# Performance work log

Measured on AMD Instinct MI355X. Metric: run time of the kernel, lower is better.

## Reference

```python
import jax, jax.numpy as jnp
import numpy as np

DT = 0.01
OMEGA_MAX = 100.0


def setup_inputs() -> dict:
    key = jax.random.key(0)
    ks = jax.random.split(key, 7)
    B, T, D, M = 4, 4096, 1024, 64
    N = 2 * M
    u = jax.random.normal(ks[0], (B, T, D), dtype=jnp.float32)
    W_omega = jax.random.normal(ks[1], (M, D), dtype=jnp.float32) * 0.02
    b_omega = jnp.ones((M,), dtype=jnp.float32)
    W_zeta = jax.random.normal(ks[2], (M, D), dtype=jnp.float32) * 0.02
    b_zeta = jnp.zeros((M,), dtype=jnp.float32)
    W_B = jax.random.normal(ks[3], (N, D), dtype=jnp.float32) * (0.1 / np.sqrt(D))
    b_B = jnp.zeros((N,), dtype=jnp.float32)
    C = jax.random.normal(ks[4], (D, N), dtype=jnp.float32) * 0.01
    D_mat = jax.random.normal(ks[5], (D, D), dtype=jnp.float32) * 0.01
    return dict(u=u, W_omega=W_omega, b_omega=b_omega, W_zeta=W_zeta,
                b_zeta=b_zeta, W_B=W_B, b_B=b_B, C=C, D_mat=D_mat)


def reference(u, W_omega, b_omega, W_zeta, b_zeta, W_B, b_B, C, D_mat):
    B, T, D = u.shape
    M = W_omega.shape[0]
    # Hoist all per-step linear projections into batched GEMMs (same math).
    omega = jax.nn.softplus(jnp.einsum('btd,md->btm', u, W_omega) + b_omega)
    omega = jnp.clip(omega, 1e-4, OMEGA_MAX)                      # (B,T,M)
    zeta = jax.nn.sigmoid(jnp.einsum('btd,md->btm', u, W_zeta) + b_zeta)
    A = omega * omega                                             # (B,T,M)
    S = 1.0 / (1.0 + (DT * DT) * A)                               # (B,T,M)
    d = 1.0 - zeta                                                # (B,T,M)
    F = jnp.einsum('btd,nd->btn', u, W_B) + b_B                   # (B,T,2M)

    def step(x, inp):
        A_t, S_t, d_t, F_t = inp                                  # (B,M)x3, (B,2M)
        z = x[:, :M]
        y = x[:, M:]
        z_new = d_t * (S_t * z - DT * A_t * S_t * y)
        y_new = d_t * (DT * S_t * z + S_t * y)
        x_new = jnp.concatenate([z_new, y_new], axis=-1) + F_t
        return x_new, x_new

    x0 = jnp.zeros((B, 2 * M), dtype=u.dtype)
    tm = lambda a: jnp.swapaxes(a, 0, 1)  # to time-major for scan
    _, xs = jax.lax.scan(step, x0, (tm(A), tm(S), tm(d), tm(F)))
    xs = jnp.swapaxes(xs, 0, 1)                                   # (B,T,2M)
    # Output projection: y_t = x_t C^T + u_t D^T
    y = jnp.einsum('btn,dn->btd', xs, C) + jnp.einsum('bte,de->btd', u, D_mat)
    return y
```

## Files before the change

kernel.cpp:

```cpp
#include <hip/hip_runtime.h>
#include <hip/hip_bf16.h>
#include <math.h>

#define DTC 0.01f

typedef __attribute__((ext_vector_type(8))) short short8;
typedef __attribute__((ext_vector_type(4))) float f32x4;
typedef unsigned short bf16raw;

__device__ __forceinline__ bf16raw f2bf(float f){
  union { unsigned u; float f; } v; v.f = f;
  unsigned r = v.u + 0x7FFF + ((v.u >> 16) & 1u);
  return (bf16raw)(r >> 16);
}

__device__ __forceinline__ short8 ld8f(const float* __restrict__ p){
  float4 a = *(const float4*)p;
  float4 b = *(const float4*)(p + 4);
  short8 r;
  r[0] = (short)f2bf(a.x); r[1] = (short)f2bf(a.y);
  r[2] = (short)f2bf(a.z); r[3] = (short)f2bf(a.w);
  r[4] = (short)f2bf(b.x); r[5] = (short)f2bf(b.y);
  r[6] = (short)f2bf(b.z); r[7] = (short)f2bf(b.w);
  return r;
}

template<int ITERS>
__device__ __forceinline__ void stage_async(const bf16raw* __restrict__ src, long ld,
                                            long row0, int k0, bf16raw* lds,
                                            int wave, int lane){
#pragma unroll
  for (int i = 0; i < ITERS; ++i){
    int r0 = (wave*ITERS + i) * 16;
    long row = row0 + r0 + (lane >> 2);
    const bf16raw* gp = src + row*ld + k0 + (lane & 3)*8;
    bf16raw* lp = lds + r0*32;
    __builtin_amdgcn_global_load_lds((const __attribute__((address_space(1))) void*)gp,
                                     (__attribute__((address_space(3))) void*)lp,
                                     16, 0, 0);
  }
}

template<int NI>
__device__ __forceinline__ void mma_tile(const bf16raw* Alds, const bf16raw* Blds,
                                         f32x4 acc[4][NI], int wm, int wn, int quad, int t16){
  short8 af[4], bfr[NI];
#pragma unroll
  for (int mi = 0; mi < 4; ++mi)
    af[mi] = *(const short8*)(Alds + (wm*64 + mi*16 + t16)*32 + quad*8);
#pragma unroll
  for (int ni = 0; ni < NI; ++ni)
    bfr[ni] = *(const short8*)(Blds + (wn*(NI*16) + ni*16 + t16)*32 + quad*8);
#pragma unroll
  for (int mi = 0; mi < 4; ++mi)
#pragma unroll
    for (int ni = 0; ni < NI; ++ni)
      acc[mi][ni] = __builtin_amdgcn_mfma_f32_16x16x32_bf16(af[mi], bfr[ni], acc[mi][ni], 0, 0, 0);
}

extern "C" __global__ void k_prep(const float* __restrict__ u,
    const float* __restrict__ Wom, const float* __restrict__ Wze,
    const float* __restrict__ WB, const float* __restrict__ Cm,
    const float* __restrict__ Dm, bf16raw* __restrict__ u_bf,
    bf16raw* __restrict__ Wcat, bf16raw* __restrict__ C_bf,
    bf16raw* __restrict__ Dm_bf){
  long g = (long)blockIdx.x * 256 + threadIdx.x;
  const float* src; bf16raw* dst; long o;
  if      (g < 2097152){ src = u;   dst = u_bf;          o = g; }
  else if (g < 2105344){ src = Wom; dst = Wcat;          o = g - 2097152; }
  else if (g < 2113536){ src = Wze; dst = Wcat + 65536;  o = g - 2105344; }
  else if (g < 2129920){ src = WB;  dst = Wcat + 131072; o = g - 2113536; }
  else if (g < 2146304){ src = Cm;  dst = C_bf;          o = g - 2129920; }
  else                 { src = Dm;  dst = Dm_bf;         o = g - 2146304; }
  *(short8*)(dst + o*8) = ld8f(src + o*8);
}

extern "C" __global__ __launch_bounds__(256) void k_gemm_p(
    const bf16raw* __restrict__ u_bf, const bf16raw* __restrict__ Wcat,
    float* __restrict__ P){
  __shared__ __align__(16) bf16raw Alds[128*32];
  __shared__ __align__(16) bf16raw Blds[128*32];
  int tid = threadIdx.x, wave = tid >> 6, lane = tid & 63;
  int quad = lane >> 4, t16 = lane & 15;
  int wm = wave >> 1, wn = wave & 1;
  long row0 = (long)blockIdx.y * 128;
  int  col0 = blockIdx.x * 128;
  f32x4 acc[4][4] = {};
  for (int kt = 0; kt < 32; ++kt){
    __syncthreads();
    stage_async<2>(u_bf, 1024, row0, kt*32, Alds, wave, lane);
    stage_async<2>(Wcat, 1024, col0, kt*32, Blds, wave, lane);
    __syncthreads();
    mma_tile<4>(Alds, Blds, acc, wm, wn, quad, t16);
  }
#pragma unroll
  for (int mi = 0; mi < 4; ++mi)
#pragma unroll
    for (int ni = 0; ni < 4; ++ni)
#pragma unroll
      for (int r = 0; r < 4; ++r){
        long grow = row0 + wm*64 + mi*16 + quad*4 + r;
        int  gcol = col0 + wn*64 + ni*16 + t16;
        P[grow*256 + gcol] = acc[mi][ni][r];
      }
}

extern "C" __global__ __launch_bounds__(256, 2) void k_gemm_out(
    const bf16raw* __restrict__ Xs, const bf16raw* __restrict__ u_bf,
    const bf16raw* __restrict__ C_bf, const bf16raw* __restrict__ Dm_bf,
    float* __restrict__ out){
  __shared__ __align__(16) bf16raw Alds[128*32];
  __shared__ __align__(16) bf16raw Blds[256*32];
  int tid = threadIdx.x, wave = tid >> 6, lane = tid & 63;
  int quad = lane >> 4, t16 = lane & 15;
  int wm = wave >> 1, wn = wave & 1;
  long row0 = (long)blockIdx.y * 128;
  int  col0 = blockIdx.x * 256;
  f32x4 acc[4][8] = {};
  for (int kt = 0; kt < 4; ++kt){
    __syncthreads();
    stage_async<2>(Xs,   128, row0, kt*32, Alds, wave, lane);
    stage_async<4>(C_bf, 128, col0, kt*32, Blds, wave, lane);
    __syncthreads();
    mma_tile<8>(Alds, Blds, acc, wm, wn, quad, t16);
  }
  for (int kt = 0; kt < 32; ++kt){
    __syncthreads();
    stage_async<2>(u_bf,  1024, row0, kt*32, Alds, wave, lane);
    stage_async<4>(Dm_bf, 1024, col0, kt*32, Blds, wave, lane);
    __syncthreads();
    mma_tile<8>(Alds, Blds, acc, wm, wn, quad, t16);
  }
#pragma unroll
  for (int mi = 0; mi < 4; ++mi)
#pragma unroll
    for (int ni = 0; ni < 8; ++ni)
#pragma unroll
      for (int r = 0; r < 4; ++r){
        long grow = row0 + wm*64 + mi*16 + quad*4 + r;
        int  gcol = col0 + wn*128 + ni*16 + t16;
        out[grow*1024 + gcol] = acc[mi][ni][r];
      }
}

extern "C" __global__ void k_coef(const float* __restrict__ P,
    const float* __restrict__ b_om, const float* __restrict__ b_ze,
    const float* __restrict__ b_B, float4* __restrict__ Coef){
  int idx = blockIdx.x * 256 + threadIdx.x;
  int bt = idx >> 6, m = idx & 63;
  const float* row = P + (size_t)bt * 256;
  float wo = row[m]       + b_om[m];
  float wz = row[64 + m]  + b_ze[m];
  float fz = row[128 + m] + b_B[m];
  float fy = row[192 + m] + b_B[64 + m];
  float sp = (wo > 20.f) ? wo : log1pf(expf(wo));
  float omega = fminf(fmaxf(sp, 1e-4f), 100.f);
  float A = omega * omega;
  float S = 1.f / (1.f + DTC*DTC*A);
  float zeta = 1.f / (1.f + expf(-wz));
  float d = 1.f - zeta;
  float p = d * S;
  float q = p * DTC * A;
  Coef[idx] = make_float4(p, q, fz, fy);
}

extern "C" __global__ void k_scan1(const float4* __restrict__ Coef,
    float4* __restrict__ CM, float2* __restrict__ CV){
  int tid = threadIdx.x, c = blockIdx.x;
  int b = tid >> 6, m = tid & 63;
  const float4* cf = Coef + ((size_t)b*4096 + c*32)*64 + m;
  float m00=1.f, m01=0.f, m10=0.f, m11=0.f, vz=0.f, vy=0.f;
#pragma unroll 4
  for (int t = 0; t < 32; ++t){
    float4 f = cf[t*64];
    float p = f.x, q = f.y;
    float nvz = p*vz - q*vy + f.z;
    float nvy = DTC*p*vz + p*vy + f.w;
    vz = nvz; vy = nvy;
    float n00 = p*m00 - q*m10;
    float n01 = p*m01 - q*m11;
    float n10 = DTC*p*m00 + p*m10;
    float n11 = DTC*p*m01 + p*m11;
    m00=n00; m01=n01; m10=n10; m11=n11;
  }
  CM[c*256 + tid] = make_float4(m00, m01, m10, m11);
  CV[c*256 + tid] = make_float2(vz, vy);
}

extern "C" __global__ void k_scan2(const float4* __restrict__ CM,
    const float2* __restrict__ CV, float2* __restrict__ XIn){
  int tid = threadIdx.x;
  float xz = 0.f, xy = 0.f;
#pragma unroll 4
  for (int c = 0; c < 128; ++c){
    XIn[c*256 + tid] = make_float2(xz, xy);
    float4 Mv = CM[c*256 + tid];
    float2 Vv = CV[c*256 + tid];
    float nz = Mv.x*xz + Mv.y*xy + Vv.x;
    float ny = Mv.z*xz + Mv.w*xy + Vv.y;
    xz = nz; xy = ny;
  }
}

extern "C" __global__ void k_scan3(const float4* __restrict__ Coef,
    const float2* __restrict__ XIn, bf16raw* __restrict__ Xs){
  int tid = threadIdx.x, c = blockIdx.x;
  int b = tid >> 6, m = tid & 63;
  const float4* cf = Coef + ((size_t)b*4096 + c*32)*64 + m;
  float2 x0 = XIn[c*256 + tid];
  float xz = x0.x, xy = x0.y;
  bf16raw* xp = Xs + ((size_t)b*4096 + c*32)*128 + m;
#pragma unroll 4
  for (int t = 0; t < 32; ++t){
    float4 f = cf[t*64];
    float p = f.x, q = f.y;
    float nz = p*xz - q*xy + f.z;
    float ny = DTC*p*xz + p*xy + f.w;
    xz = nz; xy = ny;
    xp[t*128]      = f2bf(xz);
    xp[t*128 + 64] = f2bf(xy);
  }
}

extern "C" void kernel_launch(void* const* d_in, const int* in_sizes, int n_in,
                              void* d_out, int out_size, void* d_ws, size_t ws_size,
                              hipStream_t stream){
  const float* u   = (const float*)d_in[0];
  const float* Wom = (const float*)d_in[1];
  const float* bom = (const float*)d_in[2];
  const float* Wze = (const float*)d_in[3];
  const float* bze = (const float*)d_in[4];
  const float* WB  = (const float*)d_in[5];
  const float* bB  = (const float*)d_in[6];
  const float* Cm  = (const float*)d_in[7];
  const float* Dm  = (const float*)d_in[8];
  float* out = (float*)d_out;

  char* ws = (char*)d_ws;
  size_t off = 0;
  bf16raw* u_bf  = (bf16raw*)(ws + off); off += (size_t)16777216*2;
  bf16raw* Wcat  = (bf16raw*)(ws + off); off += (size_t)262144*2;
  bf16raw* C_bf  = (bf16raw*)(ws + off); off += (size_t)131072*2;
  bf16raw* Dm_bf = (bf16raw*)(ws + off); off += (size_t)1048576*2;
  float*   P     = (float*)  (ws + off);
  bf16raw* Xs    = (bf16raw*)P;
  off += (size_t)16384*256*4;
  float4*  Coef  = (float4*) (ws + off); off += (size_t)16384*64*16;
  float4*  CMw   = (float4*) (ws + off); off += (size_t)128*256*16;
  float2*  CVw   = (float2*) (ws + off); off += (size_t)128*256*8;
  float2*  XIn   = (float2*) (ws + off); off += (size_t)128*256*8;

  k_prep    <<<8896, 256, 0, stream>>>(u, Wom, Wze, WB, Cm, Dm, u_bf, Wcat, C_bf, Dm_bf);
  k_gemm_p  <<<dim3(2, 128), 256, 0, stream>>>(u_bf, Wcat, P);
  k_coef    <<<4096, 256, 0, stream>>>(P, bom, bze, bB, Coef);
  k_scan1   <<<128, 256, 0, stream>>>(Coef, CMw, CVw);
  k_scan2   <<<1, 256, 0, stream>>>(CMw, CVw, XIn);
  k_scan3   <<<128, 256, 0, stream>>>(Coef, XIn, Xs);
  k_gemm_out<<<dim3(4, 128), 256, 0, stream>>>(Xs, u_bf, C_bf, Dm_bf, out);
}
```

Measured before the change: 233.0 us.

## Fuse u conversion into projection GEMM, merge coef+scan1, parallelize chunk scan, retile output GEMM

```diff
diff --git a/kernel.cpp b/kernel.cpp
--- a/kernel.cpp
+++ b/kernel.cpp
@@ -58,26 +58,24 @@
       acc[mi][ni] = __builtin_amdgcn_mfma_f32_16x16x32_bf16(af[mi], bfr[ni], acc[mi][ni], 0, 0, 0);
 }
 
-extern "C" __global__ void k_prep(const float* __restrict__ u,
-    const float* __restrict__ Wom, const float* __restrict__ Wze,
-    const float* __restrict__ WB, const float* __restrict__ Cm,
-    const float* __restrict__ Dm, bf16raw* __restrict__ u_bf,
+extern "C" __global__ void k_prep(const float* __restrict__ Wom,
+    const float* __restrict__ Wze, const float* __restrict__ WB,
+    const float* __restrict__ Cm, const float* __restrict__ Dm,
     bf16raw* __restrict__ Wcat, bf16raw* __restrict__ C_bf,
     bf16raw* __restrict__ Dm_bf){
   long g = (long)blockIdx.x * 256 + threadIdx.x;
   const float* src; bf16raw* dst; long o;
-  if      (g < 2097152){ src = u;   dst = u_bf;          o = g; }
-  else if (g < 2105344){ src = Wom; dst = Wcat;          o = g - 2097152; }
-  else if (g < 2113536){ src = Wze; dst = Wcat + 65536;  o = g - 2105344; }
-  else if (g < 2129920){ src = WB;  dst = Wcat + 131072; o = g - 2113536; }
-  else if (g < 2146304){ src = Cm;  dst = C_bf;          o = g - 2129920; }
-  else                 { src = Dm;  dst = Dm_bf;         o = g - 2146304; }
+  if      (g <  8192){ src = Wom; dst = Wcat;          o = g; }
+  else if (g < 16384){ src = Wze; dst = Wcat + 65536;  o = g - 8192; }
+  else if (g < 32768){ src = WB;  dst = Wcat + 131072; o = g - 16384; }
+  else if (g < 49152){ src = Cm;  dst = C_bf;          o = g - 32768; }
+  else               { src = Dm;  dst = Dm_bf;         o = g - 49152; }
   *(short8*)(dst + o*8) = ld8f(src + o*8);
 }
 
 extern "C" __global__ __launch_bounds__(256) void k_gemm_p(
-    const bf16raw* __restrict__ u_bf, const bf16raw* __restrict__ Wcat,
-    float* __restrict__ P){
+    const float* __restrict__ u, const bf16raw* __restrict__ Wcat,
+    bf16raw* __restrict__ u_bf, float* __restrict__ P){
   __shared__ __align__(16) bf16raw Alds[128*32];
   __shared__ __align__(16) bf16raw Blds[128*32];
   int tid = threadIdx.x, wave = tid >> 6, lane = tid & 63;
@@ -85,11 +83,21 @@
   int wm = wave >> 1, wn = wave & 1;
   long row0 = (long)blockIdx.y * 128;
   int  col0 = blockIdx.x * 128;
+  int srow = tid >> 2, sk = (tid & 3) * 8;
+  bool writer = (blockIdx.x == 0);
   f32x4 acc[4][4] = {};
   for (int kt = 0; kt < 32; ++kt){
-    __syncthreads();
-    stage_async<2>(u_bf, 1024, row0, kt*32, Alds, wave, lane);
-    stage_async<2>(Wcat, 1024, col0, kt*32, Blds, wave, lane);
+    int k0 = kt*32;
+    short8 a0 = ld8f(u + (row0 + srow     )*1024 + k0 + sk);
+    short8 a1 = ld8f(u + (row0 + srow + 64)*1024 + k0 + sk);
+    __syncthreads();
+    *(short8*)(Alds + (srow     )*32 + sk) = a0;
+    *(short8*)(Alds + (srow + 64)*32 + sk) = a1;
+    stage_async<2>(Wcat, 1024, col0, k0, Blds, wave, lane);
+    if (writer){
+      *(short8*)(u_bf + (row0 + srow     )*1024 + k0 + sk) = a0;
+      *(short8*)(u_bf + (row0 + srow + 64)*1024 + k0 + sk) = a1;
+    }
     __syncthreads();
     mma_tile<4>(Alds, Blds, acc, wm, wn, quad, t16);
   }
@@ -105,101 +113,88 @@
       }
 }
 
-extern "C" __global__ __launch_bounds__(256, 2) void k_gemm_out(
-    const bf16raw* __restrict__ Xs, const bf16raw* __restrict__ u_bf,
-    const bf16raw* __restrict__ C_bf, const bf16raw* __restrict__ Dm_bf,
-    float* __restrict__ out){
-  __shared__ __align__(16) bf16raw Alds[128*32];
-  __shared__ __align__(16) bf16raw Blds[256*32];
-  int tid = threadIdx.x, wave = tid >> 6, lane = tid & 63;
-  int quad = lane >> 4, t16 = lane & 15;
-  int wm = wave >> 1, wn = wave & 1;
-  long row0 = (long)blockIdx.y * 128;
-  int  col0 = blockIdx.x * 256;
-  f32x4 acc[4][8] = {};
-  for (int kt = 0; kt < 4; ++kt){
-    __syncthreads();
-    stage_async<2>(Xs,   128, row0, kt*32, Alds, wave, lane);
-    stage_async<4>(C_bf, 128, col0, kt*32, Blds, wave, lane);
-    __syncthreads();
-    mma_tile<8>(Alds, Blds, acc, wm, wn, quad, t16);
-  }
-  for (int kt = 0; kt < 32; ++kt){
-    __syncthreads();
-    stage_async<2>(u_bf,  1024, row0, kt*32, Alds, wave, lane);
-    stage_async<4>(Dm_bf, 1024, col0, kt*32, Blds, wave, lane);
-    __syncthreads();
-    mma_tile<8>(Alds, Blds, acc, wm, wn, quad, t16);
-  }
-#pragma unroll
-  for (int mi = 0; mi < 4; ++mi)
-#pragma unroll
-    for (int ni = 0; ni < 8; ++ni)
-#pragma unroll
-      for (int r = 0; r < 4; ++r){
-        long grow = row0 + wm*64 + mi*16 + quad*4 + r;
-        int  gcol = col0 + wn*128 + ni*16 + t16;
-        out[grow*1024 + gcol] = acc[mi][ni][r];
-      }
-}
-
-extern "C" __global__ void k_coef(const float* __restrict__ P,
-    const float* __restrict__ b_om, const float* __restrict__ b_ze,
-    const float* __restrict__ b_B, float4* __restrict__ Coef){
-  int idx = blockIdx.x * 256 + threadIdx.x;
-  int bt = idx >> 6, m = idx & 63;
-  const float* row = P + (size_t)bt * 256;
-  float wo = row[m]       + b_om[m];
-  float wz = row[64 + m]  + b_ze[m];
-  float fz = row[128 + m] + b_B[m];
-  float fy = row[192 + m] + b_B[64 + m];
-  float sp = (wo > 20.f) ? wo : log1pf(expf(wo));
-  float omega = fminf(fmaxf(sp, 1e-4f), 100.f);
-  float A = omega * omega;
-  float S = 1.f / (1.f + DTC*DTC*A);
-  float zeta = 1.f / (1.f + expf(-wz));
-  float d = 1.f - zeta;
-  float p = d * S;
-  float q = p * DTC * A;
-  Coef[idx] = make_float4(p, q, fz, fy);
-}
-
-extern "C" __global__ void k_scan1(const float4* __restrict__ Coef,
-    float4* __restrict__ CM, float2* __restrict__ CV){
-  int tid = threadIdx.x, c = blockIdx.x;
-  int b = tid >> 6, m = tid & 63;
-  const float4* cf = Coef + ((size_t)b*4096 + c*32)*64 + m;
-  float m00=1.f, m01=0.f, m10=0.f, m11=0.f, vz=0.f, vy=0.f;
+extern "C" __global__ __launch_bounds__(256) void k_coefscan1(
+    const float* __restrict__ P, const float* __restrict__ b_om,
+    const float* __restrict__ b_ze, const float* __restrict__ b_B,
+    float4* __restrict__ Coef, float4* __restrict__ CMt,
+    float2* __restrict__ CVt){
+  __shared__ float4 lds_c[2048];
+  int tid = threadIdx.x;
+  int c = blockIdx.x;
+  int b = blockIdx.y;
+  int t = tid >> 3;
+  int m0 = (tid & 7) * 8;
+  long bt = (long)b*4096 + c*32 + t;
+  const float* row = P + bt*256;
+#pragma unroll
+  for (int j = 0; j < 8; ++j){
+    int m = m0 + j;
+    float wo = row[m]       + b_om[m];
+    float wz = row[64 + m]  + b_ze[m];
+    float fz = row[128 + m] + b_B[m];
+    float fy = row[192 + m] + b_B[64 + m];
+    float sp = (wo > 20.f) ? wo : log1pf(expf(wo));
+    float omega = fminf(fmaxf(sp, 1e-4f), 100.f);
+    float A = omega * omega;
+    float S = 1.f / (1.f + DTC*DTC*A);
+    float zeta = 1.f / (1.f + expf(-wz));
+    float p = (1.f - zeta) * S;
+    float q = p * DTC * A;
+    float4 f4 = make_float4(p, q, fz, fy);
+    lds_c[t*64 + m] = f4;
+    Coef[bt*64 + m] = f4;
+  }
+  __syncthreads();
+  if (tid < 64){
+    int m = tid;
+    float m00=1.f, m01=0.f, m10=0.f, m11=0.f, vz=0.f, vy=0.f;
 #pragma unroll 4
-  for (int t = 0; t < 32; ++t){
-    float4 f = cf[t*64];
-    float p = f.x, q = f.y;
-    float nvz = p*vz - q*vy + f.z;
-    float nvy = DTC*p*vz + p*vy + f.w;
-    vz = nvz; vy = nvy;
-    float n00 = p*m00 - q*m10;
-    float n01 = p*m01 - q*m11;
-    float n10 = DTC*p*m00 + p*m10;
-    float n11 = DTC*p*m01 + p*m11;
-    m00=n00; m01=n01; m10=n10; m11=n11;
-  }
-  CM[c*256 + tid] = make_float4(m00, m01, m10, m11);
-  CV[c*256 + tid] = make_float2(vz, vy);
-}
-
-extern "C" __global__ void k_scan2(const float4* __restrict__ CM,
-    const float2* __restrict__ CV, float2* __restrict__ XIn){
-  int tid = threadIdx.x;
-  float xz = 0.f, xy = 0.f;
-#pragma unroll 4
-  for (int c = 0; c < 128; ++c){
-    XIn[c*256 + tid] = make_float2(xz, xy);
-    float4 Mv = CM[c*256 + tid];
-    float2 Vv = CV[c*256 + tid];
-    float nz = Mv.x*xz + Mv.y*xy + Vv.x;
-    float ny = Mv.z*xz + Mv.w*xy + Vv.y;
-    xz = nz; xy = ny;
-  }
+    for (int tt = 0; tt < 32; ++tt){
+      float4 f = lds_c[tt*64 + m];
+      float p = f.x, q = f.y;
+      float nvz = p*vz - q*vy + f.z;
+      float nvy = DTC*p*vz + p*vy + f.w;
+      vz = nvz; vy = nvy;
+      float n00 = p*m00 - q*m10;
+      float n01 = p*m01 - q*m11;
+      float n10 = DTC*p*m00 + p*m10;
+      float n11 = DTC*p*m01 + p*m11;
+      m00=n00; m01=n01; m10=n10; m11=n11;
+    }
+    int s = b*64 + m;
+    CMt[s*128 + c] = make_float4(m00, m01, m10, m11);
+    CVt[s*128 + c] = make_float2(vz, vy);
+  }
+}
+
+extern "C" __global__ __launch_bounds__(128) void k_scan2p(
+    const float4* __restrict__ CMt, const float2* __restrict__ CVt,
+    float2* __restrict__ XIn){
+  __shared__ float4 Ml[128];
+  __shared__ float2 Vl[128];
+  int c = threadIdx.x, s = blockIdx.x;
+  Ml[c] = CMt[s*128 + c];
+  Vl[c] = CVt[s*128 + c];
+  __syncthreads();
+  for (int off = 1; off < 128; off <<= 1){
+    float4 Mb; float2 Vb;
+    if (c >= off){ Mb = Ml[c-off]; Vb = Vl[c-off]; }
+    __syncthreads();
+    if (c >= off){
+      float4 Ma = Ml[c]; float2 Va = Vl[c];
+      float4 Mn; float2 Vn;
+      Mn.x = Ma.x*Mb.x + Ma.y*Mb.z;
+      Mn.y = Ma.x*Mb.y + Ma.y*Mb.w;
+      Mn.z = Ma.z*Mb.x + Ma.w*Mb.z;
+      Mn.w = Ma.z*Mb.y + Ma.w*Mb.w;
+      Vn.x = Ma.x*Vb.x + Ma.y*Vb.y + Va.x;
+      Vn.y = Ma.z*Vb.x + Ma.w*Vb.y + Va.y;
+      Ml[c] = Mn; Vl[c] = Vn;
+    }
+    __syncthreads();
+  }
+  float2 xin = (c == 0) ? make_float2(0.f, 0.f) : Vl[c-1];
+  XIn[c*256 + s] = xin;
 }
 
 extern "C" __global__ void k_scan3(const float4* __restrict__ Coef,
@@ -222,6 +217,44 @@
   }
 }
 
+extern "C" __global__ __launch_bounds__(256) void k_gemm_out(
+    const bf16raw* __restrict__ Xs, const bf16raw* __restrict__ u_bf,
+    const bf16raw* __restrict__ C_bf, const bf16raw* __restrict__ Dm_bf,
+    float* __restrict__ out){
+  __shared__ __align__(16) bf16raw Alds[128*32];
+  __shared__ __align__(16) bf16raw Blds[128*32];
+  int tid = threadIdx.x, wave = tid >> 6, lane = tid & 63;
+  int quad = lane >> 4, t16 = lane & 15;
+  int wm = wave >> 1, wn = wave & 1;
+  long row0 = (long)blockIdx.y * 128;
+  int  col0 = blockIdx.x * 128;
+  f32x4 acc[4][4] = {};
+  for (int kt = 0; kt < 4; ++kt){
+    __syncthreads();
+    stage_async<2>(Xs,   128, row0, kt*32, Alds, wave, lane);
+    stage_async<2>(C_bf, 128, col0, kt*32, Blds, wave, lane);
+    __syncthreads();
+    mma_tile<4>(Alds, Blds, acc, wm, wn, quad, t16);
+  }
+  for (int kt = 0; kt < 32; ++kt){
+    __syncthreads();
+    stage_async<2>(u_bf,  1024, row0, kt*32, Alds, wave, lane);
+    stage_async<2>(Dm_bf, 1024, col0, kt*32, Blds, wave, lane);
+    __syncthreads();
+    mma_tile<4>(Alds, Blds, acc, wm, wn, quad, t16);
+  }
+#pragma unroll
+  for (int mi = 0; mi < 4; ++mi)
+#pragma unroll
+    for (int ni = 0; ni < 4; ++ni)
+#pragma unroll
+      for (int r = 0; r < 4; ++r){
+        long grow = row0 + wm*64 + mi*16 + quad*4 + r;
+        int  gcol = col0 + wn*64 + ni*16 + t16;
+        out[grow*1024 + gcol] = acc[mi][ni][r];
+      }
+}
+
 extern "C" void kernel_launch(void* const* d_in, const int* in_sizes, int n_in,
                               void* d_out, int out_size, void* d_ws, size_t ws_size,
                               hipStream_t stream){
@@ -246,15 +279,14 @@
   bf16raw* Xs    = (bf16raw*)P;
   off += (size_t)16384*256*4;
   float4*  Coef  = (float4*) (ws + off); off += (size_t)16384*64*16;
-  float4*  CMw   = (float4*) (ws + off); off += (size_t)128*256*16;
-  float2*  CVw   = (float2*) (ws + off); off += (size_t)128*256*8;
+  float4*  CMt   = (float4*) (ws + off); off += (size_t)256*128*16;
+  float2*  CVt   = (float2*) (ws + off); off += (size_t)256*128*8;
   float2*  XIn   = (float2*) (ws + off); off += (size_t)128*256*8;
 
-  k_prep    <<<8896, 256, 0, stream>>>(u, Wom, Wze, WB, Cm, Dm, u_bf, Wcat, C_bf, Dm_bf);
-  k_gemm_p  <<<dim3(2, 128), 256, 0, stream>>>(u_bf, Wcat, P);
-  k_coef    <<<4096, 256, 0, stream>>>(P, bom, bze, bB, Coef);
-  k_scan1   <<<128, 256, 0, stream>>>(Coef, CMw, CVw);
-  k_scan2   <<<1, 256, 0, stream>>>(CMw, CVw, XIn);
-  k_scan3   <<<128, 256, 0, stream>>>(Coef, XIn, Xs);
-  k_gemm_out<<<dim3(4, 128), 256, 0, stream>>>(Xs, u_bf, C_bf, Dm_bf, out);
-}
+  k_prep     <<<704, 256, 0, stream>>>(Wom, Wze, WB, Cm, Dm, Wcat, C_bf, Dm_bf);
+  k_gemm_p   <<<dim3(2, 128), 256, 0, stream>>>(u, Wcat, u_bf, P);
+  k_coefscan1<<<dim3(128, 4), 256, 0, stream>>>(P, bom, bze, bB, Coef, CMt, CVt);
+  k_scan2p   <<<256, 128, 0, stream>>>(CMt, CVt, XIn);
+  k_scan3    <<<128, 256, 0, stream>>>(Coef, XIn, Xs);
+  k_gemm_out <<<dim3(8, 128), 256, 0, stream>>>(Xs, u_bf, C_bf, Dm_bf, out);
+}
```

Result: slower. 273.7 us (+17.5%).
